# Performance work log

Hardware: AMD Instinct MI355X
Metric: run time of the kernel (lower is better)

The kernel has to match this reference:

```python
import jax, jax.numpy as jnp
import numpy as np

B, T, C, H, N = 4, 1024, 2048, 32, 64
DFF, DW, DV, DA, DG = 8192, 64, 32, 64, 128
GN_EPS = 64e-5  # RWKV7 ln_x GroupNorm eps


def _ln(x, w, b, eps=1e-5):
    m = x.mean(-1, keepdims=True)
    v = ((x - m) ** 2).mean(-1, keepdims=True)
    return (x - m) / jnp.sqrt(v + eps) * w + b


def _block(x, v_first, att_shift, ffn_shift, wkv_state,
           ln1_w, ln1_b, ln2_w, ln2_b,
           x_r, x_w, x_k, x_v, x_a, x_g,
           Wr, Wk, Wv, Wo,
           w0, w1, w2, v0, v1, v2, a0, a1, a2, g1, g2,
           k_k, k_a, r_k, lnx_w, lnx_b,
           ffn_xk, Wk_ffn, Wv_ffn):
    # ----- TimeMix -----
    xn = _ln(x, ln1_w, ln1_b)
    xx = jnp.concatenate([att_shift[:, None, :], xn[:, :-1]], axis=1) - xn
    xr = xn + xx * x_r
    xw = xn + xx * x_w
    xk_ = xn + xx * x_k
    xv = xn + xx * x_v
    xa = xn + xx * x_a
    xg = xn + xx * x_g

    r = xr @ Wr
    w = -jax.nn.softplus(-(w0 + jnp.tanh(xw @ w1) @ w2)) - 0.5  # <= -0.5
    k = xk_ @ Wk
    v = xv @ Wv
    # layer_id != 0: interpolate toward v_first
    v = v + (v_first - v) * jax.nn.sigmoid(v0 + (xv @ v1) @ v2)
    a = jax.nn.sigmoid(a0 + (xa @ a1) @ a2)
    g = jax.nn.sigmoid(xg @ g1) @ g2

    kk = (k * k_k).reshape(B, T, H, N)
    kk = kk / jnp.maximum(jnp.linalg.norm(kk, axis=-1, keepdims=True), 1e-12)
    k = k * (1.0 + (a - 1.0) * k_a)

    rh = r.reshape(B, T, H, N)
    wh = jnp.exp(-jnp.exp(w.reshape(B, T, H, N)))  # decay in (0,1)
    kh = k.reshape(B, T, H, N)
    vh = v.reshape(B, T, H, N)
    ah = a.reshape(B, T, H, N)
    aa = -kk
    bb = kk * ah

    def step(S, inp):
        # S: [B,H,N(value),N(key)]
        r_t, w_t, k_t, v_t, a_t, b_t = inp
        sa = jnp.einsum('bhvk,bhk->bhv', S, a_t)
        S = S * w_t[:, :, None, :] + sa[..., None] * b_t[:, :, None, :] + v_t[..., None] * k_t[:, :, None, :]
        y = jnp.einsum('bhvk,bhk->bhv', S, r_t)
        return S, y

    tm = lambda z: jnp.swapaxes(z, 0, 1)  # [B,T,H,N] -> [T,B,H,N]
    S_new, ys = jax.lax.scan(step, wkv_state, (tm(rh), tm(wh), tm(kh), tm(vh), tm(aa), tm(bb)))
    x_wkv = jnp.swapaxes(ys, 0, 1).reshape(B, T, C)

    # GroupNorm over H groups of size N (RWKV7 ln_x)
    xh = x_wkv.reshape(B, T, H, N)
    mu = xh.mean(-1, keepdims=True)
    var = ((xh - mu) ** 2).mean(-1, keepdims=True)
    x_wkv = ((xh - mu) / jnp.sqrt(var + GN_EPS)).reshape(B, T, C) * lnx_w + lnx_b

    resid = ((rh * kh * r_k).sum(-1, keepdims=True) * vh).reshape(B, T, C)
    x_wkv = x_wkv + resid
    att_out = (x_wkv * g) @ Wo
    x1 = x + att_out

    # ----- ChannelMix -----
    xn2 = _ln(x1, ln2_w, ln2_b)
    xx2 = jnp.concatenate([ffn_shift[:, None, :], xn2[:, :-1]], axis=1) - xn2
    xkf = xn2 + xx2 * ffn_xk
    kf = jnp.square(jax.nn.relu(xkf @ Wk_ffn))
    x_out = x1 + kf @ Wv_ffn
    return x_out, S_new


def setup_inputs() -> dict:
    ks = jax.random.split(jax.random.key(0), 48)
    rn = lambda i, sh, s=1.0: jax.random.normal(ks[i], sh, dtype=jnp.float32) * s
    return {
        'x': rn(0, (B, T, C)), 'v_first': rn(1, (B, T, C)),
        'att_shift': rn(2, (B, C)), 'ffn_shift': rn(3, (B, C)),
        'wkv_state': jnp.zeros((B, H, N, N), jnp.float32),
        'ln1_w': jnp.ones((C,), jnp.float32), 'ln1_b': jnp.zeros((C,), jnp.float32),
        'ln2_w': jnp.ones((C,), jnp.float32), 'ln2_b': jnp.zeros((C,), jnp.float32),
        'x_r': rn(4, (C,), 0.3), 'x_w': rn(5, (C,), 0.3), 'x_k': rn(6, (C,), 0.3),
        'x_v': rn(7, (C,), 0.3), 'x_a': rn(8, (C,), 0.3), 'x_g': rn(9, (C,), 0.3),
        'Wr': rn(10, (C, C), 0.02), 'Wk': rn(11, (C, C), 0.02),
        'Wv': rn(12, (C, C), 0.02), 'Wo': rn(13, (C, C), 0.02),
        'w0': rn(14, (C,), 0.3), 'w1': rn(15, (C, DW), 0.02), 'w2': rn(16, (DW, C), 0.02),
        'v0': rn(17, (C,), 0.3), 'v1': rn(18, (C, DV), 0.02), 'v2': rn(19, (DV, C), 0.02),
        'a0': rn(20, (C,), 0.3), 'a1': rn(21, (C, DA), 0.02), 'a2': rn(22, (DA, C), 0.02),
        'g1': rn(23, (C, DG), 0.02), 'g2': rn(24, (DG, C), 0.02),
        'k_k': rn(25, (C,), 0.1) + 0.7, 'k_a': rn(26, (C,), 0.1) + 0.7, 'r_k': rn(27, (H, N), 0.1),
        'lnx_w': jnp.ones((C,), jnp.float32), 'lnx_b': jnp.zeros((C,), jnp.float32),
        'ffn_xk': rn(28, (C,), 0.3), 'Wk_ffn': rn(29, (C, DFF), 0.02), 'Wv_ffn': rn(30, (DFF, C), 0.02),
    }


def reference(x, v_first, att_shift, ffn_shift, wkv_state,
              ln1_w, ln1_b, ln2_w, ln2_b,
              x_r, x_w, x_k, x_v, x_a, x_g,
              Wr, Wk, Wv, Wo,
              w0, w1, w2, v0, v1, v2, a0, a1, a2, g1, g2,
              k_k, k_a, r_k, lnx_w, lnx_b,
              ffn_xk, Wk_ffn, Wv_ffn):
    return _block(x, v_first, att_shift, ffn_shift, wkv_state,
                  ln1_w, ln1_b, ln2_w, ln2_b,
                  x_r, x_w, x_k, x_v, x_a, x_g,
                  Wr, Wk, Wv, Wo,
                  w0, w1, w2, v0, v1, v2, a0, a1, a2, g1, g2,
                  k_k, k_a, r_k, lnx_w, lnx_b,
                  ffn_xk, Wk_ffn, Wv_ffn)
```

## Files before the change

kernel.cpp:

```cpp
#include <hip/hip_runtime.h>
#include <cstdint>


typedef __attribute__((ext_vector_type(4))) float f32x4;
typedef __attribute__((ext_vector_type(8))) __bf16 bf16x8;
typedef __attribute__((ext_vector_type(8))) unsigned short us8;

#define DEV __device__ __forceinline__

DEV unsigned short f2b(float f) {
  union { float f; unsigned u; } v; v.f = f;
  unsigned r = v.u + 0x7fffu + ((v.u >> 16) & 1u);
  return (unsigned short)(r >> 16);
}
DEV float b2f(unsigned short u) {
  union { unsigned u; float f; } v; v.u = (unsigned)u << 16;
  return v.f;
}

DEV void gload16(const void* g, void* l) {
  void* gg = const_cast<void*>(g);
  __builtin_amdgcn_global_load_lds(
      (__attribute__((address_space(1))) unsigned int*)gg,
      (__attribute__((address_space(3))) unsigned int*)l, 16, 0, 0);
}

DEV float red8(float v) {
  v += __shfl_xor(v, 1);
  v += __shfl_xor(v, 2);
  v += __shfl_xor(v, 4);
  return v;
}


__global__ void k_transpose(const float* __restrict__ src,
                            unsigned short* __restrict__ dst, int R, int Cc) {
  __shared__ float tile[32][33];
  const int c0 = blockIdx.x * 32, r0 = blockIdx.y * 32;
  const int tx = threadIdx.x, ty = threadIdx.y;
  for (int i = ty; i < 32; i += 8)
    tile[i][tx] = src[(size_t)(r0 + i) * Cc + c0 + tx];
  __syncthreads();
  for (int i = ty; i < 32; i += 8)
    dst[(size_t)(c0 + i) * R + r0 + tx] = f2b(tile[tx][i]);
}

__global__ void k_wcat(const float* __restrict__ w1, const float* __restrict__ a1,
                       const float* __restrict__ v1, const float* __restrict__ g1,
                       const float* __restrict__ xw, const float* __restrict__ xa,
                       const float* __restrict__ xv, const float* __restrict__ xg,
                       unsigned short* __restrict__ dst) {
  const int i = blockIdx.x * 256 + threadIdx.x;
  if (i >= 384 * 4096) return;
  const int j = i >> 12, c = i & 4095;
  float val = 0.f;
  if (j < 288) {
    const float* W; const float* mix; int jj, D;
    if (j < 64)       { W = w1; mix = xw; jj = j;       D = 64;  }
    else if (j < 128) { W = a1; mix = xa; jj = j - 64;  D = 64;  }
    else if (j < 160) { W = v1; mix = xv; jj = j - 128; D = 32;  }
    else              { W = g1; mix = xg; jj = j - 160; D = 128; }
    const int cc = c & 2047;
    val = W[(size_t)cc * D + jj];
    if (c >= 2048) val *= mix[cc];
  }
  dst[i] = f2b(val);
}

__global__ void k_wup(const float* __restrict__ w2, const float* __restrict__ a2,
                      const float* __restrict__ v2, const float* __restrict__ g2,
                      unsigned short* __restrict__ dst) {
  const int i = blockIdx.x * 256 + threadIdx.x;
  if (i >= 8192 * 288) return;
  const int n = i / 288, k = i - n * 288;
  const int p = n >> 11, j = n & 2047;
  float val = 0.f;
  if (p == 0)      { if (k < 64)              val = w2[(size_t)k * 2048 + j]; }
  else if (p == 1) { if (k >= 64 && k < 128)  val = a2[(size_t)(k - 64) * 2048 + j]; }
  else if (p == 2) { if (k >= 128 && k < 160) val = v2[(size_t)(k - 128) * 2048 + j]; }
  else             { if (k >= 160)            val = g2[(size_t)(k - 160) * 2048 + j]; }
  dst[i] = f2b(val);
}


DEV void breduce2(float& a, float& b, float* rbuf) {
#pragma unroll
  for (int m = 1; m < 64; m <<= 1) { a += __shfl_xor(a, m); b += __shfl_xor(b, m); }
  const int wid = threadIdx.x >> 6, lane = threadIdx.x & 63;
  if (lane == 0) { rbuf[wid] = a; rbuf[4 + wid] = b; }
  __syncthreads();
  a = rbuf[0] + rbuf[1] + rbuf[2] + rbuf[3];
  b = rbuf[4] + rbuf[5] + rbuf[6] + rbuf[7];
  __syncthreads();
}

__global__ __launch_bounds__(256)
void k_ln1_mix(const float* __restrict__ x, const float* __restrict__ shift,
               const float* __restrict__ lw, const float* __restrict__ lb,
               const float* __restrict__ mr, const float* __restrict__ mk,
               const float* __restrict__ mv,
               unsigned short* __restrict__ A2, unsigned short* __restrict__ xrb,
               unsigned short* __restrict__ xkb, unsigned short* __restrict__ xvb) {
  __shared__ float rbuf[8];
  const int m = blockIdx.x, tid = threadIdx.x;
  const int b = m >> 10, t = m & 1023;
  const float* xt = x + (size_t)m * 2048 + tid * 8;
  const float* xp = (t > 0) ? (x + (size_t)(m - 1) * 2048 + tid * 8)
                            : (shift + (size_t)b * 2048 + tid * 8);
  float vt[8], vp[8];
  *(float4*)&vt[0] = *(const float4*)(xt);
  *(float4*)&vt[4] = *(const float4*)(xt + 4);
  *(float4*)&vp[0] = *(const float4*)(xp);
  *(float4*)&vp[4] = *(const float4*)(xp + 4);
  float st = 0.f, sp = 0.f;
#pragma unroll
  for (int i = 0; i < 8; ++i) { st += vt[i]; sp += vp[i]; }
  breduce2(st, sp, rbuf);
  const float mt_ = st * (1.f / 2048.f), mp_ = sp * (1.f / 2048.f);
  float qt = 0.f, qp = 0.f;
#pragma unroll
  for (int i = 0; i < 8; ++i) {
    float d0 = vt[i] - mt_; qt += d0 * d0;
    float d1 = vp[i] - mp_; qp += d1 * d1;
  }
  breduce2(qt, qp, rbuf);
  const float rt = rsqrtf(qt * (1.f / 2048.f) + 1e-5f);
  const float rp = rsqrtf(qp * (1.f / 2048.f) + 1e-5f);
  const bool lnp = (t > 0);
#pragma unroll
  for (int i = 0; i < 8; ++i) {
    const int c = tid * 8 + i;
    const float wv = lw[c], bv = lb[c];
    const float xn = (vt[i] - mt_) * rt * wv + bv;
    const float pn = lnp ? ((vp[i] - mp_) * rp * wv + bv) : vp[i];
    const float xx = pn - xn;
    A2[(size_t)m * 4096 + c] = f2b(xn);
    A2[(size_t)m * 4096 + 2048 + c] = f2b(xx);
    xrb[(size_t)m * 2048 + c] = f2b(xn + xx * mr[c]);
    xkb[(size_t)m * 2048 + c] = f2b(xn + xx * mk[c]);
    xvb[(size_t)m * 2048 + c] = f2b(xn + xx * mv[c]);
  }
}

__global__ __launch_bounds__(256)
void k_ln2_mix(const float* __restrict__ x1, const float* __restrict__ shift,
               const float* __restrict__ lw, const float* __restrict__ lb,
               const float* __restrict__ mk, unsigned short* __restrict__ xkf) {
  __shared__ float rbuf[8];
  const int m = blockIdx.x, tid = threadIdx.x;
  const int b = m >> 10, t = m & 1023;
  const float* xt = x1 + (size_t)m * 2048 + tid * 8;
  const float* xp = (t > 0) ? (x1 + (size_t)(m - 1) * 2048 + tid * 8)
                            : (shift + (size_t)b * 2048 + tid * 8);
  float vt[8], vp[8];
  *(float4*)&vt[0] = *(const float4*)(xt);
  *(float4*)&vt[4] = *(const float4*)(xt + 4);
  *(float4*)&vp[0] = *(const float4*)(xp);
  *(float4*)&vp[4] = *(const float4*)(xp + 4);
  float st = 0.f, sp = 0.f;
#pragma unroll
  for (int i = 0; i < 8; ++i) { st += vt[i]; sp += vp[i]; }
  breduce2(st, sp, rbuf);
  const float mt_ = st * (1.f / 2048.f), mp_ = sp * (1.f / 2048.f);
  float qt = 0.f, qp = 0.f;
#pragma unroll
  for (int i = 0; i < 8; ++i) {
    float d0 = vt[i] - mt_; qt += d0 * d0;
    float d1 = vp[i] - mp_; qp += d1 * d1;
  }
  breduce2(qt, qp, rbuf);
  const float rt = rsqrtf(qt * (1.f / 2048.f) + 1e-5f);
  const float rp = rsqrtf(qp * (1.f / 2048.f) + 1e-5f);
  const bool lnp = (t > 0);
#pragma unroll
  for (int i = 0; i < 8; ++i) {
    const int c = tid * 8 + i;
    const float wv = lw[c], bv = lb[c];
    const float xn = (vt[i] - mt_) * rt * wv + bv;
    const float pn = lnp ? ((vp[i] - mp_) * rp * wv + bv) : vp[i];
    xkf[(size_t)m * 2048 + c] = f2b(xn + (pn - xn) * mk[c]);
  }
}


constexpr int EP_F32 = 0, EP_B16 = 1, EP_RELU2 = 5, EP_ADDF = 6, EP_HACT = 7;

template <int EP>
DEV void ep_store(float acc, long row, long c, long ldc, float* Co,
                  unsigned short* Cob, const float* bias, const float* e0f,
                  const unsigned short* e0b) {
  const long idx = row * ldc + c;
  (void)bias; (void)e0b;
  if constexpr (EP == EP_F32) {
    Co[idx] = acc;
  } else if constexpr (EP == EP_B16) {
    Cob[idx] = f2b(acc);
  } else if constexpr (EP == EP_RELU2) {
    const float r = fmaxf(acc, 0.f);
    Cob[idx] = f2b(r * r);
  } else if constexpr (EP == EP_ADDF) {
    Co[idx] = acc + e0f[idx];
  } else if constexpr (EP == EP_HACT) {
    float vv = acc;
    if (c < 64) vv = tanhf(vv);
    else if (c >= 160) vv = 1.f / (1.f + expf(-vv));
    Cob[idx] = f2b(vv);
  }
}


template <int EP>
__global__ __launch_bounds__(256)
void gemm_bt(const unsigned short* __restrict__ A, long lda,
             const unsigned short* __restrict__ Bt, long ldb, long N, long K,
             long ldc, float* __restrict__ Co, unsigned short* __restrict__ Cob,
             const float* __restrict__ bias, const float* __restrict__ e0f,
             const unsigned short* __restrict__ e0b) {
  __shared__ unsigned short As[4096];
  __shared__ unsigned short Bs[4096];
  const int tid = threadIdx.x;
  const int wid = tid >> 6, lane = tid & 63;
  const long row0 = (long)blockIdx.x * 128, col0 = (long)blockIdx.y * 128;
  const int wm = (wid >> 1) * 64, wn = (wid & 1) * 64;
  f32x4 acc[4][4] = {};
  const int sr = tid >> 2, sk = (tid & 3) * 8;
  const unsigned short* gA = A + (row0 + sr) * lda + sk;
  const unsigned short* gB = Bt + (col0 + sr) * ldb + sk;
  unsigned short* lA = As + wid * 512;
  unsigned short* lB = Bs + wid * 512;
  const int fr = lane & 15, fk = (lane >> 4) * 8;

  for (long kb = 0; kb < K; kb += 32) {
    gload16(gA + kb, lA);
    gload16(gA + kb + 64 * lda, lA + 2048);
    gload16(gB + kb, lB);
    gload16(gB + kb + 64 * ldb, lB + 2048);
    __syncthreads();
    bf16x8 af[4], bq[4];
#pragma unroll
    for (int mt = 0; mt < 4; ++mt)
      af[mt] = *(const bf16x8*)(As + (wm + mt * 16 + fr) * 32 + fk);
#pragma unroll
    for (int nt = 0; nt < 4; ++nt)
      bq[nt] = *(const bf16x8*)(Bs + (wn + nt * 16 + fr) * 32 + fk);
#pragma unroll
    for (int mt = 0; mt < 4; ++mt)
#pragma unroll
      for (int nt = 0; nt < 4; ++nt)
        acc[mt][nt] = __builtin_amdgcn_mfma_f32_16x16x32_bf16(
            af[mt], bq[nt], acc[mt][nt], 0, 0, 0);
    __syncthreads();
  }
  const int fq = lane >> 4;
#pragma unroll
  for (int mt = 0; mt < 4; ++mt) {
#pragma unroll
    for (int nt = 0; nt < 4; ++nt) {
      const long c = col0 + wn + nt * 16 + fr;
      if (c < N) {
        const long rb = row0 + wm + mt * 16 + fq * 4;
#pragma unroll
        for (int rg = 0; rg < 4; ++rg)
          ep_store<EP>(acc[mt][nt][rg], rb + rg, c, ldc, Co, Cob, bias, e0f, e0b);
      }
    }
  }
}


template <int EP>
__global__ __launch_bounds__(256)
void gemm3(const unsigned short* __restrict__ A, long lda,
           const unsigned short* __restrict__ Bt, long ldb, long K, long ldc,
           float* __restrict__ Co, unsigned short* __restrict__ Cob,
           const float* __restrict__ e0f) {
  __shared__ unsigned short As[2][4096];
  __shared__ unsigned short Bs[2][4096];
  const int tid = threadIdx.x;
  const int wid = tid >> 6, lane = tid & 63;
  const long row0 = (long)blockIdx.x * 128, col0 = (long)blockIdx.y * 128;
  const int wm = (wid >> 1) * 64, wn = (wid & 1) * 64;
  f32x4 acc[4][4] = {};
  const int srow = tid >> 2;
  const int scol = 8 * ((tid & 3) ^ (srow & 3));
  const unsigned short* gA = A + (row0 + srow) * lda + scol;
  const unsigned short* gB = Bt + (col0 + srow) * ldb + scol;
  const int fr = lane & 15, fc = lane >> 4;

#define STAGE3(buf, kb)                                         \
  {                                                             \
    gload16(gA + (kb), &As[buf][0] + wid * 512);                \
    gload16(gA + (kb) + 64 * lda, &As[buf][2048] + wid * 512);  \
    gload16(gB + (kb), &Bs[buf][0] + wid * 512);                \
    gload16(gB + (kb) + 64 * ldb, &Bs[buf][2048] + wid * 512);  \
  }

  STAGE3(0, 0)
  const int NT = (int)(K >> 5);
  int cur = 0;
  for (int kt = 0; kt < NT; ++kt) {
    if (kt + 1 < NT) {
      STAGE3(cur ^ 1, (long)(kt + 1) * 32)
      asm volatile("s_waitcnt vmcnt(4)" ::: "memory");
    } else {
      asm volatile("s_waitcnt vmcnt(0)" ::: "memory");
    }
    __builtin_amdgcn_s_barrier();
    asm volatile("" ::: "memory");
    bf16x8 af[4], bq[4];
#pragma unroll
    for (int mt = 0; mt < 4; ++mt) {
      const int r = wm + mt * 16 + fr;
      af[mt] = *(const bf16x8*)(&As[cur][0] + r * 32 + ((fc ^ (r & 3)) * 8));
    }
#pragma unroll
    for (int nt = 0; nt < 4; ++nt) {
      const int r = wn + nt * 16 + fr;
      bq[nt] = *(const bf16x8*)(&Bs[cur][0] + r * 32 + ((fc ^ (r & 3)) * 8));
    }
    __builtin_amdgcn_s_setprio(1);
#pragma unroll
    for (int mt = 0; mt < 4; ++mt)
#pragma unroll
      for (int nt = 0; nt < 4; ++nt)
        acc[mt][nt] = __builtin_amdgcn_mfma_f32_16x16x32_bf16(
            af[mt], bq[nt], acc[mt][nt], 0, 0, 0);
    __builtin_amdgcn_s_setprio(0);
    asm volatile("" ::: "memory");
    __builtin_amdgcn_s_barrier();
    cur ^= 1;
  }
#undef STAGE3
  const int fq = lane >> 4;
#pragma unroll
  for (int mt = 0; mt < 4; ++mt) {
#pragma unroll
    for (int nt = 0; nt < 4; ++nt) {
      const long c = col0 + wn + nt * 16 + fr;
      const long rb = row0 + wm + mt * 16 + fq * 4;
#pragma unroll
      for (int rg = 0; rg < 4; ++rg)
        ep_store<EP>(acc[mt][nt][rg], rb + rg, c, ldc, Co, Cob, nullptr, e0f,
                     nullptr);
    }
  }
}


__global__ __launch_bounds__(256)
void gemm_up128(const unsigned short* __restrict__ A,
                const unsigned short* __restrict__ Bt,
                float* __restrict__ whb, unsigned short* __restrict__ abuf,
                unsigned short* __restrict__ vfb, unsigned short* __restrict__ gbuf,
                const float* __restrict__ w0, const float* __restrict__ a0,
                const float* __restrict__ v0,
                const unsigned short* __restrict__ vraw,
                const float* __restrict__ vfirst) {
  __shared__ unsigned short As[2][4096];
  __shared__ unsigned short Bs[2][4096];
  const int tid = threadIdx.x;
  const int wid = tid >> 6, lane = tid & 63;
  const long row0 = (long)blockIdx.x * 128, col0 = (long)blockIdx.y * 128;
  const int wm = (wid >> 1) * 64, wn = (wid & 1) * 64;
  f32x4 acc[4][4] = {};
  const int srow = tid >> 2;
  const int scol = 8 * ((tid & 3) ^ (srow & 3));
  const unsigned short* gA = A + (row0 + srow) * 288 + scol;
  const unsigned short* gB = Bt + (col0 + srow) * 288 + scol;
  const int fr = lane & 15, fc = lane >> 4;

#define STAGEU(buf, kb)                                         \
  {                                                             \
    gload16(gA + (kb), &As[buf][0] + wid * 512);                \
    gload16(gA + (kb) + 64 * 288, &As[buf][2048] + wid * 512);  \
    gload16(gB + (kb), &Bs[buf][0] + wid * 512);                \
    gload16(gB + (kb) + 64 * 288, &Bs[buf][2048] + wid * 512);  \
  }

  STAGEU(0, 0)
  int cur = 0;
  for (int kt = 0; kt < 9; ++kt) {
    if (kt + 1 < 9) {
      STAGEU(cur ^ 1, (long)(kt + 1) * 32)
      asm volatile("s_waitcnt vmcnt(4)" ::: "memory");
    } else {
      asm volatile("s_waitcnt vmcnt(0)" ::: "memory");
    }
    __builtin_amdgcn_s_barrier();
    asm volatile("" ::: "memory");
    bf16x8 af[4], bq[4];
#pragma unroll
    for (int mt = 0; mt < 4; ++mt) {
      const int r = wm + mt * 16 + fr;
      af[mt] = *(const bf16x8*)(&As[cur][0] + r * 32 + ((fc ^ (r & 3)) * 8));
    }
#pragma unroll
    for (int nt = 0; nt < 4; ++nt) {
      const int r = wn + nt * 16 + fr;
      bq[nt] = *(const bf16x8*)(&Bs[cur][0] + r * 32 + ((fc ^ (r & 3)) * 8));
    }
    __builtin_amdgcn_s_setprio(1);
#pragma unroll
    for (int mt = 0; mt < 4; ++mt)
#pragma unroll
      for (int nt = 0; nt < 4; ++nt)
        acc[mt][nt] = __builtin_amdgcn_mfma_f32_16x16x32_bf16(
            af[mt], bq[nt], acc[mt][nt], 0, 0, 0);
    __builtin_amdgcn_s_setprio(0);
    asm volatile("" ::: "memory");
    __builtin_amdgcn_s_barrier();
    cur ^= 1;
  }
#undef STAGEU
  const int fq = lane >> 4;
  const int p = (int)(blockIdx.y >> 4);
#pragma unroll
  for (int mt = 0; mt < 4; ++mt) {
#pragma unroll
    for (int nt = 0; nt < 4; ++nt) {
      const long c = col0 + wn + nt * 16 + fr;
      const long cc = c & 2047;
      const long rb = row0 + wm + mt * 16 + fq * 4;
#pragma unroll
      for (int rg = 0; rg < 4; ++rg) {
        const float av = acc[mt][nt][rg];
        const long idx = (rb + rg) * 2048 + cc;
        if (p == 0) {
          const float wv = w0[cc] + av;
          const float sp = log1pf(expf(-wv));
          whb[idx] = expf(-expf(-sp - 0.5f));
        } else if (p == 1) {
          abuf[idx] = f2b(1.f / (1.f + expf(-(a0[cc] + av))));
        } else if (p == 2) {
          const float s = 1.f / (1.f + expf(-(v0[cc] + av)));
          const float vv = b2f(vraw[idx]);
          vfb[idx] = f2b(vv + (vfirst[idx] - vv) * s);
        } else {
          gbuf[idx] = f2b(av);
        }
      }
    }
  }
}

__global__ __launch_bounds__(256)
void k_post(unsigned short* __restrict__ kio, unsigned short* __restrict__ abio,
            unsigned short* __restrict__ aao, const float* __restrict__ kkw,
            const float* __restrict__ kaw) {
  const int m = blockIdx.x, tid = threadIdx.x;
  const size_t base = (size_t)m * 2048 + tid * 8;
  us8 k8 = *(const us8*)(kio + base);
  us8 a8 = *(const us8*)(abio + base);
  float kk8[8], ka8[8];
  *(float4*)&kk8[0] = *(const float4*)(kkw + tid * 8);
  *(float4*)&kk8[4] = *(const float4*)(kkw + tid * 8 + 4);
  *(float4*)&ka8[0] = *(const float4*)(kaw + tid * 8);
  *(float4*)&ka8[4] = *(const float4*)(kaw + tid * 8 + 4);
  float kx[8], kv[8], av[8];
  float ss = 0.f;
#pragma unroll
  for (int i = 0; i < 8; ++i) {
    kv[i] = b2f(k8[i]); av[i] = b2f(a8[i]);
    kx[i] = kv[i] * kk8[i]; ss += kx[i] * kx[i];
  }
  ss = red8(ss);
  const float inv = 1.f / fmaxf(sqrtf(ss), 1e-12f);
  us8 kh8, aa8, bb8;
#pragma unroll
  for (int i = 0; i < 8; ++i) {
    const float kkn = kx[i] * inv;
    kh8[i] = f2b(kv[i] * (1.f + (av[i] - 1.f) * ka8[i]));
    aa8[i] = f2b(-kkn);
    bb8[i] = f2b(kkn * av[i]);
  }
  *(us8*)(kio + base) = kh8;
  *(us8*)(aao + base) = aa8;
  *(us8*)(abio + base) = bb8;
}


DEV float red16(float x) {
  union { float f; int i; } a, r;
  a.f = x; r.i = __builtin_amdgcn_update_dpp(0, a.i, 0xB1, 0xf, 0xf, true);
  x += r.f;
  a.f = x; r.i = __builtin_amdgcn_update_dpp(0, a.i, 0x4E, 0xf, 0xf, true);
  x += r.f;
  a.f = x; r.i = __builtin_amdgcn_update_dpp(0, a.i, 0x124, 0xf, 0xf, true);
  x += r.f;
  a.f = x; r.i = __builtin_amdgcn_update_dpp(0, a.i, 0x128, 0xf, 0xf, true);
  x += r.f;
  return x;
}

DEV void cv4(const uint2 q, float* o) {
  union { unsigned u; float f; } t;
  t.u = q.x << 16;          o[0] = t.f;
  t.u = q.x & 0xffff0000u;  o[1] = t.f;
  t.u = q.y << 16;          o[2] = t.f;
  t.u = q.y & 0xffff0000u;  o[3] = t.f;
}

__global__ __launch_bounds__(64)
void k_scan(const unsigned short* __restrict__ rp,
            const unsigned short* __restrict__ kp,
            const unsigned short* __restrict__ vp,
            const float* __restrict__ wp,
            const unsigned short* __restrict__ ap,
            const unsigned short* __restrict__ bp,
            const float* __restrict__ s0, unsigned short* __restrict__ yout,
            float* __restrict__ snew) {
  __shared__ float4 slots[8][49];
  __shared__ unsigned short ylds[1024][4];
  const int lane = threadIdx.x;
  const int bh = blockIdx.x & 127;
  const int rq = blockIdx.x >> 7;
  const int b = bh >> 5, h = bh & 31;
  const int kg = lane & 15, rl = lane >> 4;
  const int v = rq * 4 + rl, ks = kg * 4;
  const size_t off_bh = (size_t)b * 1024 * 2048 + (size_t)h * 64;
  const int vfo = 768 + ((rq & 1) * 4 + rl) * 2;

  float S[4];
  *(float4*)&S[0] = *(const float4*)(s0 + (((size_t)bh * 64 + v) * 64 + ks));

  const char* gp = nullptr;
  size_t gstep = 0;
  if (lane < 49) {
    if (lane < 32) {
      const int arr = lane >> 3, sub = lane & 7;
      const unsigned short* base = arr == 0 ? rp : arr == 1 ? kp
                                 : arr == 2 ? ap : bp;
      gp = (const char*)(base + off_bh + sub * 8);
      gstep = 4096;
    } else if (lane < 48) {
      gp = (const char*)(wp + off_bh + (lane - 32) * 4);
      gstep = 8192;
    } else {
      gp = (const char*)(vp + off_bh + (rq & ~1) * 4);
      gstep = 4096;
    }
  }
#pragma unroll
  for (int s = 0; s < 8; ++s) {
    if (lane < 49) gload16(gp, &slots[s][0]);
    gp += gstep;
  }

  uint2 rA, kA, aA, bA, rB, kB, aB, bB;
  float4 wA, wB;
  unsigned short fA, fB;
  asm volatile("s_waitcnt vmcnt(7)" ::: "memory");
  {
    const char* nb = (const char*)&slots[0][0];
    rA = *(const uint2*)(nb + kg * 8);
    kA = *(const uint2*)(nb + 128 + kg * 8);
    aA = *(const uint2*)(nb + 256 + kg * 8);
    bA = *(const uint2*)(nb + 384 + kg * 8);
    wA = *(const float4*)(nb + 512 + kg * 16);
    fA = *(const unsigned short*)(nb + vfo);
  }

#define SSTEP(T, Cr, Ck, Ca, Cb, Cw, Cf, Nr, Nk, Na, Nb, Nw, Nf)             \
  {                                                                          \
    asm volatile("s_waitcnt lgkmcnt(0)" ::: "memory");                       \
    if (lane < 49) gload16(gp, &slots[(T) & 7][0]);                          \
    if ((T) < 1015) gp += gstep;                                             \
    asm volatile("s_waitcnt vmcnt(7)" ::: "memory");                         \
    const char* nb = (const char*)&slots[((T) + 1) & 7][0];                  \
    Nr = *(const uint2*)(nb + kg * 8);                                       \
    Nk = *(const uint2*)(nb + 128 + kg * 8);                                 \
    Na = *(const uint2*)(nb + 256 + kg * 8);                                 \
    Nb = *(const uint2*)(nb + 384 + kg * 8);                                 \
    Nw = *(const float4*)(nb + 512 + kg * 16);                               \
    Nf = *(const unsigned short*)(nb + vfo);                                 \
    float rr[4], kk[4], av[4], bv[4];                                        \
    cv4(Cr, rr); cv4(Ck, kk); cv4(Ca, av); cv4(Cb, bv);                      \
    const float vv = b2f(Cf);                                                \
    float sa = S[0] * av[0] + S[1] * av[1] + S[2] * av[2] + S[3] * av[3];    \
    sa = red16(sa);                                                          \
    float y;                                                                 \
    S[0] = S[0] * Cw.x + sa * bv[0] + vv * kk[0]; y  = S[0] * rr[0];         \
    S[1] = S[1] * Cw.y + sa * bv[1] + vv * kk[1]; y += S[1] * rr[1];         \
    S[2] = S[2] * Cw.z + sa * bv[2] + vv * kk[2]; y += S[2] * rr[2];         \
    S[3] = S[3] * Cw.w + sa * bv[3] + vv * kk[3]; y += S[3] * rr[3];         \
    y = red16(y);                                                            \
    if (kg == 0) ylds[T][rl] = f2b(y);                                       \
  }

  for (int tb = 0; tb < 1024; tb += 2) {
    SSTEP(tb + 0, rA, kA, aA, bA, wA, fA, rB, kB, aB, bB, wB, fB)
    SSTEP(tb + 1, rB, kB, aB, bB, wB, fB, rA, kA, aA, bA, wA, fA)
  }
#undef SSTEP

  *(float4*)(snew + (((size_t)bh * 64 + v) * 64 + ks)) = *(const float4*)&S[0];
  asm volatile("s_waitcnt lgkmcnt(0)" ::: "memory");
#pragma unroll 4
  for (int it = 0; it < 16; ++it) {
    const int t = lane + it * 64;
    const uint2 val = *(const uint2*)&ylds[t][0];
    *(uint2*)(yout + off_bh + (size_t)t * 2048 + rq * 4) = val;
  }
}


__global__ __launch_bounds__(256)
void k_gn(const unsigned short* __restrict__ y, const unsigned short* __restrict__ r,
          const unsigned short* __restrict__ kh, const unsigned short* __restrict__ vf,
          const unsigned short* __restrict__ g, const float* __restrict__ rk,
          const float* __restrict__ lw, const float* __restrict__ lb,
          unsigned short* __restrict__ ywg) {
  const int m = blockIdx.x, tid = threadIdx.x;
  const size_t base = (size_t)m * 2048 + tid * 8;
  us8 y8 = *(const us8*)(y + base);
  us8 r8 = *(const us8*)(r + base);
  us8 k8 = *(const us8*)(kh + base);
  us8 v8 = *(const us8*)(vf + base);
  us8 g8 = *(const us8*)(g + base);
  float yv[8];
  float rkv[8];
  *(float4*)&rkv[0] = *(const float4*)(rk + tid * 8);
  *(float4*)&rkv[4] = *(const float4*)(rk + tid * 8 + 4);
  float sy = 0.f, sd = 0.f;
#pragma unroll
  for (int i = 0; i < 8; ++i) {
    yv[i] = b2f(y8[i]);
    sy += yv[i];
    sd += b2f(r8[i]) * b2f(k8[i]) * rkv[i];
  }
  sy = red8(sy);
  sd = red8(sd);
  const float mu = sy * (1.f / 64.f);
  float sq = 0.f;
#pragma unroll
  for (int i = 0; i < 8; ++i) { const float d = yv[i] - mu; sq += d * d; }
  sq = red8(sq);
  const float rstd = rsqrtf(sq * (1.f / 64.f) + 64e-5f);
  us8 o8;
#pragma unroll
  for (int i = 0; i < 8; ++i) {
    const int c = tid * 8 + i;
    const float gn = (yv[i] - mu) * rstd * lw[c] + lb[c];
    o8[i] = f2b((gn + sd * b2f(v8[i])) * b2f(g8[i]));
  }
  *(us8*)(ywg + base) = o8;
}


extern "C" void kernel_launch(void* const* d_in, const int* in_sizes, int n_in,
                              void* d_out, int out_size, void* d_ws,
                              size_t ws_size, hipStream_t stream) {
  (void)in_sizes; (void)n_in; (void)out_size; (void)ws_size;
  const float* x         = (const float*)d_in[0];
  const float* v_first   = (const float*)d_in[1];
  const float* att_shift = (const float*)d_in[2];
  const float* ffn_shift = (const float*)d_in[3];
  const float* wkv0      = (const float*)d_in[4];
  const float* ln1w = (const float*)d_in[5];
  const float* ln1b = (const float*)d_in[6];
  const float* ln2w = (const float*)d_in[7];
  const float* ln2b = (const float*)d_in[8];
  const float* x_r = (const float*)d_in[9];
  const float* x_w = (const float*)d_in[10];
  const float* x_k = (const float*)d_in[11];
  const float* x_v = (const float*)d_in[12];
  const float* x_a = (const float*)d_in[13];
  const float* x_g = (const float*)d_in[14];
  const float* Wr = (const float*)d_in[15];
  const float* Wk = (const float*)d_in[16];
  const float* Wv = (const float*)d_in[17];
  const float* Wo = (const float*)d_in[18];
  const float* w0 = (const float*)d_in[19];
  const float* w1 = (const float*)d_in[20];
  const float* w2 = (const float*)d_in[21];
  const float* v0 = (const float*)d_in[22];
  const float* v1 = (const float*)d_in[23];
  const float* v2 = (const float*)d_in[24];
  const float* a0 = (const float*)d_in[25];
  const float* a1 = (const float*)d_in[26];
  const float* a2 = (const float*)d_in[27];
  const float* g1 = (const float*)d_in[28];
  const float* g2 = (const float*)d_in[29];
  const float* k_k = (const float*)d_in[30];
  const float* k_a = (const float*)d_in[31];
  const float* r_k = (const float*)d_in[32];
  const float* lnxw = (const float*)d_in[33];
  const float* lnxb = (const float*)d_in[34];
  const float* ffn_xk = (const float*)d_in[35];
  const float* Wkf = (const float*)d_in[36];
  const float* Wvf = (const float*)d_in[37];

  char* ws = (char*)d_ws;
  constexpr size_t OFF_TWR   = 0;
  constexpr size_t OFF_TWK   = 8388608;
  constexpr size_t OFF_TWV   = 16777216;
  constexpr size_t OFF_TWO   = 25165824;
  constexpr size_t OFF_TWCAT = 34734080;
  constexpr size_t OFF_HACT  = 37879808;
  constexpr size_t OFF_GBUF  = 40239104;
  constexpr size_t OFF_WH    = 57016320;
  constexpr size_t OFF_R     = 90570752;
  constexpr size_t OFF_KH    = 107347968;
  constexpr size_t OFF_VF    = 124125184;
  constexpr size_t OFF_AA    = 140902400;
  constexpr size_t OFF_BB    = 157679616;
  constexpr size_t OFF_TWUP  = 174456832;

  unsigned short* tWr = (unsigned short*)(ws + OFF_TWR);
  unsigned short* tWk = (unsigned short*)(ws + OFF_TWK);
  unsigned short* tWv = (unsigned short*)(ws + OFF_TWV);
  unsigned short* tWo = (unsigned short*)(ws + OFF_TWO);
  unsigned short* tWcat = (unsigned short*)(ws + OFF_TWCAT);
  unsigned short* Hact  = (unsigned short*)(ws + OFF_HACT);
  unsigned short* gbuf  = (unsigned short*)(ws + OFF_GBUF);
  unsigned short* tWvfh = (unsigned short*)(ws + OFF_GBUF);
  unsigned short* act2  = (unsigned short*)(ws + OFF_WH);
  float*          whb   = (float*)(ws + OFF_WH);
  unsigned short* ywg   = (unsigned short*)(ws + OFF_WH);
  unsigned short* kf    = (unsigned short*)(ws + OFF_WH);
  unsigned short* bxr   = (unsigned short*)(ws + OFF_AA);
  unsigned short* bxk   = (unsigned short*)(ws + OFF_BB);
  unsigned short* bxv   = (unsigned short*)(ws + OFF_VF);
  unsigned short* rbuf  = (unsigned short*)(ws + OFF_R);
  unsigned short* khb   = (unsigned short*)(ws + OFF_KH);
  unsigned short* vfb   = (unsigned short*)(ws + OFF_VF);
  unsigned short* aab   = (unsigned short*)(ws + OFF_AA);
  unsigned short* bbb   = (unsigned short*)(ws + OFF_BB);
  unsigned short* vraw  = (unsigned short*)(ws + OFF_AA);
  unsigned short* abuf  = (unsigned short*)(ws + OFF_BB);
  float*          x1    = (float*)(ws + OFF_R);
  unsigned short* xkf   = (unsigned short*)(ws + OFF_VF);
  unsigned short* tWkf  = (unsigned short*)(ws + OFF_AA);
  unsigned short* tWup  = (unsigned short*)(ws + OFF_TWUP);
  float* out = (float*)d_out;
  float* snew = out + 8388608;

  const dim3 tb(32, 8);
  k_transpose<<<dim3(64, 64), tb, 0, stream>>>(Wr, tWr, 2048, 2048);
  k_transpose<<<dim3(64, 64), tb, 0, stream>>>(Wk, tWk, 2048, 2048);
  k_transpose<<<dim3(64, 64), tb, 0, stream>>>(Wv, tWv, 2048, 2048);
  k_transpose<<<dim3(64, 64), tb, 0, stream>>>(Wo, tWo, 2048, 2048);
  k_wcat<<<6144, 256, 0, stream>>>(w1, a1, v1, g1, x_w, x_a, x_v, x_g, tWcat);
  k_wup<<<9216, 256, 0, stream>>>(w2, a2, v2, g2, tWup);

  k_ln1_mix<<<4096, 256, 0, stream>>>(x, att_shift, ln1w, ln1b, x_r, x_k, x_v,
                                      act2, bxr, bxk, bxv);
  gemm3<EP_B16><<<dim3(32, 16), 256, 0, stream>>>(
      bxr, 2048, tWr, 2048, 2048, 2048, nullptr, rbuf, nullptr);
  gemm3<EP_B16><<<dim3(32, 16), 256, 0, stream>>>(
      bxk, 2048, tWk, 2048, 2048, 2048, nullptr, khb, nullptr);
  gemm3<EP_B16><<<dim3(32, 16), 256, 0, stream>>>(
      bxv, 2048, tWv, 2048, 2048, 2048, nullptr, vraw, nullptr);
  gemm_bt<EP_HACT><<<dim3(32, 3), 256, 0, stream>>>(
      act2, 4096, tWcat, 4096, 288, 4096, 288, nullptr, Hact, nullptr, nullptr, nullptr);
  gemm_up128<<<dim3(32, 64), 256, 0, stream>>>(
      Hact, tWup, whb, abuf, vfb, gbuf, w0, a0, v0, vraw, v_first);
  k_post<<<4096, 256, 0, stream>>>(khb, abuf, aab, k_k, k_a);

  k_scan<<<2048, 64, 0, stream>>>(rbuf, khb, vfb, whb, aab, bbb, wkv0,
                                  (unsigned short*)out, snew);
  k_gn<<<4096, 256, 0, stream>>>((const unsigned short*)out, rbuf, khb, vfb,
                                 gbuf, r_k, lnxw, lnxb, ywg);

  gemm3<EP_ADDF><<<dim3(32, 16), 256, 0, stream>>>(
      ywg, 2048, tWo, 2048, 2048, 2048, x1, nullptr, x);

  k_ln2_mix<<<4096, 256, 0, stream>>>(x1, ffn_shift, ln2w, ln2b, ffn_xk, xkf);
  k_transpose<<<dim3(256, 64), tb, 0, stream>>>(Wkf, tWkf, 2048, 8192);
  gemm3<EP_RELU2><<<dim3(32, 32), 256, 0, stream>>>(
      xkf, 2048, tWkf, 2048, 2048, 4096, nullptr, kf, nullptr);
  k_transpose<<<dim3(64, 128), tb, 0, stream>>>(Wvf, tWvfh, 4096, 2048);
  gemm3<EP_ADDF><<<dim3(32, 16), 256, 0, stream>>>(
      kf, 4096, tWvfh, 4096, 4096, 2048, out, nullptr, x1);
  gemm3<EP_RELU2><<<dim3(32, 32), 256, 0, stream>>>(
      xkf, 2048, tWkf + (size_t)4096 * 2048, 2048, 2048, 4096, nullptr, kf, nullptr);
  k_transpose<<<dim3(64, 128), tb, 0, stream>>>(Wvf + (size_t)4096 * 2048, tWvfh,
                                                4096, 2048);
  gemm3<EP_ADDF><<<dim3(32, 16), 256, 0, stream>>>(
      kf, 4096, tWvfh, 4096, 4096, 2048, out, nullptr, out);
}
```

Baseline: 1.286 ms.

## Add 256x256-tile 8-wave GEMM with phased staging for FFN up-projection

Adds a new GEMM kernel with 256x256 output tiles, 512 threads (8 waves) and 128KB of LDS double buffering. It stages the four 128-row halves of A and B in separate phases that are interleaved with MFMA work, using partial vmcnt waits and setprio. It replaces the 128x128 gemm3 for the two FFN key (ReLU^2) GEMMs, with the aim of raising data reuse per byte loaded and overlapping global loads with compute. The trade-off is fewer blocks (256 per launch) and heavy LDS use that limits occupancy to one block per CU.

```diff
diff --git a/kernel.cpp b/kernel.cpp
--- a/kernel.cpp
+++ b/kernel.cpp
@@ -344,6 +344,114 @@
                      nullptr);
     }
   }
+}
+
+
+template <int EP>
+__global__ __launch_bounds__(512)
+void gemm8p(const unsigned short* __restrict__ A, long lda,
+            const unsigned short* __restrict__ Bt, long ldb, long K, long ldc,
+            float* __restrict__ Co, unsigned short* __restrict__ Cob,
+            const float* __restrict__ e0f) {
+  __shared__ unsigned short lds[65536];
+  const int tid = threadIdx.x;
+  const int wid = tid >> 6, lane = tid & 63;
+  const long row0 = (long)blockIdx.x * 256, col0 = (long)blockIdx.y * 256;
+  const int wrow = (wid >> 2) * 64;
+  const int wcol = (wid & 3) * 32;
+  const int fr = lane & 15, fc = lane >> 4;
+  f32x4 acc[2][4][2][2] = {};
+
+  const int sr0 = tid >> 3;
+  int sce = (tid & 7) * 8;
+  sce ^= ((sr0 >> 2) & 1) << 4;
+  const unsigned short* gA = A + (row0 + sr0) * lda + sce;
+  const unsigned short* gB = Bt + (col0 + sr0) * ldb + sce;
+
+#define STG8(half, src, ld, kb, buf)                                     \
+  {                                                                      \
+    const unsigned short* s_ = (src) + (kb);                             \
+    unsigned short* d_ = lds + (buf) * 32768 + (half) * 8192 + tid * 8;  \
+    gload16(s_, d_);                                                     \
+    gload16(s_ + 64 * (ld), d_ + 4096);                                  \
+  }
+
+  STG8(0, gA, lda, 0, 0)
+  STG8(2, gB, ldb, 0, 0)
+  STG8(1, gA + 128 * lda, lda, 0, 0)
+  STG8(3, gB + 128 * ldb, ldb, 0, 0)
+  asm volatile("s_waitcnt vmcnt(0)" ::: "memory");
+  __builtin_amdgcn_s_barrier();
+
+  const int NT = (int)(K >> 6);
+  int cur = 0;
+
+#define PHASE8(P, KT)                                                         \
+  {                                                                           \
+    constexpr int mh = (P) >> 1, nh = (P) & 1;                                \
+    const int bb = cur * 32768;                                               \
+    bf16x8 af[4][2], bq[2][2];                                                \
+    _Pragma("unroll") for (int mt = 0; mt < 4; ++mt)                          \
+      _Pragma("unroll") for (int ks = 0; ks < 2; ++ks) {                      \
+        const int r = wrow + mt * 16 + fr;                                    \
+        const int e = (ks * 32 + fc * 8) ^ (((r >> 2) & 1) << 4);             \
+        af[mt][ks] = *(const bf16x8*)(lds + bb + mh * 8192 + r * 64 + e);     \
+      }                                                                       \
+    _Pragma("unroll") for (int nt = 0; nt < 2; ++nt)                          \
+      _Pragma("unroll") for (int ks = 0; ks < 2; ++ks) {                      \
+        const int r = wcol + nt * 16 + fr;                                    \
+        const int e = (ks * 32 + fc * 8) ^ (((r >> 2) & 1) << 4);             \
+        bq[nt][ks] =                                                          \
+            *(const bf16x8*)(lds + bb + 16384 + nh * 8192 + r * 64 + e);      \
+      }                                                                       \
+    if ((KT) + 1 < NT) {                                                      \
+      const long kb_ = (long)((KT) + 1) * 64;                                 \
+      if constexpr ((P) == 0) STG8(0, gA, lda, kb_, cur ^ 1)                  \
+      else if constexpr ((P) == 1) STG8(2, gB, ldb, kb_, cur ^ 1)             \
+      else if constexpr ((P) == 2) STG8(1, gA + 128 * lda, lda, kb_, cur ^ 1) \
+      else STG8(3, gB + 128 * ldb, ldb, kb_, cur ^ 1)                         \
+    }                                                                         \
+    if constexpr ((P) == 0) asm volatile("s_waitcnt vmcnt(2)" ::: "memory");  \
+    if constexpr ((P) == 3) asm volatile("s_waitcnt vmcnt(4)" ::: "memory");  \
+    __builtin_amdgcn_s_barrier();                                             \
+    asm volatile("s_waitcnt lgkmcnt(0)" ::: "memory");                        \
+    __builtin_amdgcn_s_setprio(1);                                            \
+    _Pragma("unroll") for (int mt = 0; mt < 4; ++mt)                          \
+      _Pragma("unroll") for (int nt = 0; nt < 2; ++nt)                        \
+        _Pragma("unroll") for (int ks = 0; ks < 2; ++ks)                      \
+          acc[mh][mt][nh][nt] = __builtin_amdgcn_mfma_f32_16x16x32_bf16(      \
+              af[mt][ks], bq[nt][ks], acc[mh][mt][nh][nt], 0, 0, 0);          \
+    __builtin_amdgcn_s_setprio(0);                                            \
+    asm volatile("" ::: "memory");                                            \
+    __builtin_amdgcn_s_barrier();                                             \
+  }
+
+  for (int kt = 0; kt < NT; ++kt) {
+    PHASE8(0, kt)
+    PHASE8(1, kt)
+    PHASE8(2, kt)
+    PHASE8(3, kt)
+    cur ^= 1;
+  }
+#undef PHASE8
+#undef STG8
+
+  const int fq = lane >> 4;
+#pragma unroll
+  for (int mh = 0; mh < 2; ++mh)
+#pragma unroll
+    for (int mt = 0; mt < 4; ++mt)
+#pragma unroll
+      for (int nh = 0; nh < 2; ++nh)
+#pragma unroll
+        for (int nt = 0; nt < 2; ++nt) {
+          const long c = col0 + nh * 128 + wcol + nt * 16 + fr;
+          const long rb = row0 + mh * 128 + wrow + mt * 16 + fq * 4;
+#pragma unroll
+          for (int rg = 0; rg < 4; ++rg)
+            ep_store<EP>(acc[mh][mt][nh][nt][rg], rb + rg, c, ldc, Co, Cob,
+                         nullptr, e0f, nullptr);
+        }
 }
 
 
@@ -767,12 +875,12 @@
 
   k_ln2_mix<<<4096, 256, 0, stream>>>(x1, ffn_shift, ln2w, ln2b, ffn_xk, xkf);
   k_transpose<<<dim3(256, 64), tb, 0, stream>>>(Wkf, tWkf, 2048, 8192);
-  gemm3<EP_RELU2><<<dim3(32, 32), 256, 0, stream>>>(
+  gemm8p<EP_RELU2><<<dim3(16, 16), 512, 0, stream>>>(
       xkf, 2048, tWkf, 2048, 2048, 4096, nullptr, kf, nullptr);
   k_transpose<<<dim3(64, 128), tb, 0, stream>>>(Wvf, tWvfh, 4096, 2048);
   gemm3<EP_ADDF><<<dim3(32, 16), 256, 0, stream>>>(
       kf, 4096, tWvfh, 4096, 4096, 2048, out, nullptr, x1);
-  gemm3<EP_RELU2><<<dim3(32, 32), 256, 0, stream>>>(
+  gemm8p<EP_RELU2><<<dim3(16, 16), 512, 0, stream>>>(
       xkf, 2048, tWkf + (size_t)4096 * 2048, 2048, 2048, 4096, nullptr, kf, nullptr);
   k_transpose<<<dim3(64, 128), tb, 0, stream>>>(Wvf + (size_t)4096 * 2048, tWvfh,
                                                 4096, 2048);
```

After: 1.276 ms. About the same (-0.8%).
